# Kernel optimization log

Hardware: AMD Instinct MI355X
Metric: run time of the kernel (lower is better)

Reference implementation:

```python
import jax, jax.numpy as jnp
import numpy as np

HEADS = 16

def setup_inputs() -> dict:
    key = jax.random.key(0)
    k1, k2, k3, k4 = jax.random.split(key, 4)
    B, T, S, W = 2, 2048, 2048, 1024
    x = jax.random.normal(k1, (B, T, W), dtype=jnp.float32)
    cond_k = jax.random.normal(k2, (B, S, W), dtype=jnp.float32)
    cond_v = jax.random.normal(k3, (B, S, W), dtype=jnp.float32)
    w_proj = jax.random.normal(k4, (W, W), dtype=jnp.float32) * 0.02
    b_proj = jnp.zeros((W,), dtype=jnp.float32)
    return {"x": x, "cond_k": cond_k, "cond_v": cond_v, "w_proj": w_proj, "b_proj": b_proj}

def reference(x, cond_k, cond_v, w_proj, b_proj):
    B, T, W = x.shape
    S = cond_k.shape[1]
    H = HEADS
    d = W // H
    scale = 1.0 / jnp.sqrt(jnp.sqrt(jnp.float32(d)))  # applied to both q and k
    q = x.reshape(B, T, H, d) * scale
    k = cond_k.reshape(B, S, H, d) * scale
    v = cond_v.reshape(B, S, H, d)
    # scores: [B, H, T, S]
    scores = jnp.einsum('bthd,bshd->bhts', q, k)
    w = jax.nn.softmax(scores.astype(jnp.float32), axis=-1).astype(scores.dtype)
    out = jnp.einsum('bhts,bshd->bthd', w, v).reshape(B, T, W)
    # c_proj: torch Linear -> x @ W.T + b
    return out @ w_proj.T + b_proj
```

## Files before the change

### kernel.cpp

```cpp
#include <hip/hip_runtime.h>

#define Bn 2
#define Hn 16
#define Tn 2048
#define Sn 2048
#define Wd 1024
#define Dh 64

typedef __attribute__((ext_vector_type(8))) short s16x8;
typedef __attribute__((ext_vector_type(4))) short s16x4;
typedef __attribute__((ext_vector_type(4))) float f32x4;
typedef __attribute__((ext_vector_type(4))) unsigned u32x4;

#define MFMA(a, b, c) __builtin_amdgcn_mfma_f32_16x16x32_bf16((a), (b), (c), 0, 0, 0)

__device__ __forceinline__ s16x8 ld8(const short* p) { return *(const s16x8*)p; }

__device__ __forceinline__ short f2bf(float f) {
    unsigned u = __builtin_bit_cast(unsigned, f);
    u += 0x7FFFu + ((u >> 16) & 1u);
    return (short)(u >> 16);
}

__device__ __forceinline__ unsigned cvtpk(float lo, float hi) {
    unsigned r;
    asm("v_cvt_pk_bf16_f32 %0, %1, %2" : "=v"(r) : "v"(lo), "v"(hi));
    return r;
}

__global__ void cvt_scale(const float* __restrict__ in, short* __restrict__ out,
                          int n, float s) {
    int i = (blockIdx.x * 256 + threadIdx.x) * 8;
    if (i < n) {
        float4 a = *(const float4*)(in + i);
        float4 b = *(const float4*)(in + i + 4);
        s16x8 o;
        o[0] = f2bf(a.x * s); o[1] = f2bf(a.y * s); o[2] = f2bf(a.z * s); o[3] = f2bf(a.w * s);
        o[4] = f2bf(b.x * s); o[5] = f2bf(b.y * s); o[6] = f2bf(b.z * s); o[7] = f2bf(b.w * s);
        *(s16x8*)(out + i) = o;
    }
}

__global__ __launch_bounds__(256) void vtrans(const float* __restrict__ cv,
                                              short* __restrict__ vt) {
    __shared__ short T[64][68];
    const int st = blockIdx.x & 31;
    const int bh = blockIdx.x >> 5;
    const int b = bh >> 4, h = bh & 15;
    const int tid = threadIdx.x;
#pragma unroll
    for (int i = 0; i < 4; ++i) {
        int f = i * 256 + tid, sr = f >> 4, c4 = f & 15;
        float4 v = *(const float4*)(cv + (size_t)(b * Sn + st * 64 + sr) * Wd + h * Dh + c4 * 4);
        s16x4 o;
        o[0] = f2bf(v.x); o[1] = f2bf(v.y); o[2] = f2bf(v.z); o[3] = f2bf(v.w);
        *(s16x4*)&T[sr][c4 * 4] = o;
    }
    __syncthreads();
#pragma unroll
    for (int i = 0; i < 4; ++i) {
        int f = i * 256 + tid, dr = f >> 4, p4 = f & 15;
        s16x4 o;
#pragma unroll
        for (int k = 0; k < 4; ++k) {
            int sl = ((p4 >> 3) * 2 + (p4 & 1)) * 16 + ((p4 >> 1) & 3) * 4 + k;
            o[k] = T[sl][dr];
        }
        *(s16x4*)(vt + (size_t)(bh * Dh + dr) * Sn + st * 64 + p4 * 4) = o;
    }
}

#define KSTR 72

__global__ __launch_bounds__(256, 2) void attn_fused(
    const float* __restrict__ x, const short* __restrict__ kb,
    const short* __restrict__ vt, short* __restrict__ ao)
{
    __shared__ alignas(16) short Ks[2][64 * KSTR];
    __shared__ alignas(16) short Vs[2][64 * KSTR];

    const int tid  = threadIdx.x;
    const int w    = tid >> 6;
    const int l    = tid & 63;
    const int quad = l >> 4;
    const int l16  = l & 15;

    const int bh = blockIdx.x & 31;
    const int qt = blockIdx.x >> 5;
    const int b  = bh >> 4, h = bh & 15;

    const int qrow0 = qt * 128 + w * 32;

    const float SQ = 0.125f * 1.4426950408889634f;
    s16x8 aq[2][2];
#pragma unroll
    for (int mi = 0; mi < 2; ++mi)
#pragma unroll
        for (int c = 0; c < 2; ++c) {
            const float* p = x + (size_t)(b * Tn + qrow0 + mi * 16 + l16) * Wd
                               + h * Dh + c * 32 + quad * 8;
            float4 a = ((const float4*)p)[0], bb = ((const float4*)p)[1];
            s16x8 o;
            o[0] = f2bf(a.x * SQ); o[1] = f2bf(a.y * SQ); o[2] = f2bf(a.z * SQ); o[3] = f2bf(a.w * SQ);
            o[4] = f2bf(bb.x * SQ); o[5] = f2bf(bb.y * SQ); o[6] = f2bf(bb.z * SQ); o[7] = f2bf(bb.w * SQ);
            aq[mi][c] = o;
        }

    f32x4 oacc[2][4];
    float dn[2];
#pragma unroll
    for (int mi = 0; mi < 2; ++mi) {
#pragma unroll
        for (int nt = 0; nt < 4; ++nt) {
            oacc[mi][nt][0] = 0.f; oacc[mi][nt][1] = 0.f;
            oacc[mi][nt][2] = 0.f; oacc[mi][nt][3] = 0.f;
        }
        dn[mi] = 0.f;
    }

    const short* kb_h = kb + (size_t)(b * Sn) * Wd + h * Dh;
    const short* vt_h = vt + (size_t)(bh * Dh) * Sn;

    const int sr = tid >> 3;
    const int sg = tid & 7;

    s16x8 kr[2], vr[2];
#pragma unroll
    for (int i = 0; i < 2; ++i) {
        int r0 = sr + i * 32;
        kr[i] = ld8(kb_h + (size_t)r0 * Wd + sg * 8);
        vr[i] = ld8(vt_h + (size_t)r0 * Sn + sg * 8);
    }
#pragma unroll
    for (int i = 0; i < 2; ++i) {
        int r0 = sr + i * 32;
        *(s16x8*)&Ks[0][r0 * KSTR + sg * 8] = kr[i];
        *(s16x8*)&Vs[0][r0 * KSTR + sg * 8] = vr[i];
    }
    __syncthreads();

    const int NIT = Sn / 64;
    for (int it = 0; it < NIT; ++it) {
        const int p = it & 1;

        if (it + 1 < NIT) {
            const int s1 = (it + 1) * 64;
#pragma unroll
            for (int i = 0; i < 2; ++i) {
                int r0 = sr + i * 32;
                kr[i] = ld8(kb_h + (size_t)(s1 + r0) * Wd + sg * 8);
                vr[i] = ld8(vt_h + (size_t)r0 * Sn + s1 + sg * 8);
            }
        }

        f32x4 sc[2][4];
        const f32x4 z = {0.f, 0.f, 0.f, 0.f};
        __builtin_amdgcn_s_setprio(1);
#pragma unroll
        for (int sj = 0; sj < 4; ++sj) {
            s16x8 k0 = *(const s16x8*)&Ks[p][(sj * 16 + l16) * KSTR + quad * 8];
            s16x8 k1 = *(const s16x8*)&Ks[p][(sj * 16 + l16) * KSTR + 32 + quad * 8];
#pragma unroll
            for (int mi = 0; mi < 2; ++mi) {
                sc[mi][sj] = MFMA(k0, aq[mi][0], z);
                sc[mi][sj] = MFMA(k1, aq[mi][1], sc[mi][sj]);
            }
        }
        __builtin_amdgcn_s_setprio(0);

        s16x8 ap[2][2];
#pragma unroll
        for (int mi = 0; mi < 2; ++mi) {
            float ex[4][4];
#pragma unroll
            for (int sj = 0; sj < 4; ++sj)
#pragma unroll
                for (int r = 0; r < 4; ++r)
                    ex[sj][r] = __builtin_amdgcn_exp2f(sc[mi][sj][r]);
            dn[mi] += (((ex[0][0] + ex[0][1]) + (ex[0][2] + ex[0][3]))
                     + ((ex[1][0] + ex[1][1]) + (ex[1][2] + ex[1][3])))
                    + (((ex[2][0] + ex[2][1]) + (ex[2][2] + ex[2][3]))
                     + ((ex[3][0] + ex[3][1]) + (ex[3][2] + ex[3][3])));
#pragma unroll
            for (int g = 0; g < 2; ++g) {
                u32x4 pk;
                pk[0] = cvtpk(ex[2 * g][0],     ex[2 * g][1]);
                pk[1] = cvtpk(ex[2 * g][2],     ex[2 * g][3]);
                pk[2] = cvtpk(ex[2 * g + 1][0], ex[2 * g + 1][1]);
                pk[3] = cvtpk(ex[2 * g + 1][2], ex[2 * g + 1][3]);
                ap[mi][g] = __builtin_bit_cast(s16x8, pk);
            }
        }

        s16x8 bv[4][2];
#pragma unroll
        for (int nt = 0; nt < 4; ++nt)
#pragma unroll
            for (int g = 0; g < 2; ++g)
                bv[nt][g] = *(const s16x8*)&Vs[p][(nt * 16 + l16) * KSTR + g * 32 + quad * 8];
        __builtin_amdgcn_s_setprio(1);
#pragma unroll
        for (int mi = 0; mi < 2; ++mi)
#pragma unroll
            for (int nt = 0; nt < 4; ++nt) {
                oacc[mi][nt] = MFMA(ap[mi][0], bv[nt][0], oacc[mi][nt]);
                oacc[mi][nt] = MFMA(ap[mi][1], bv[nt][1], oacc[mi][nt]);
            }
        __builtin_amdgcn_s_setprio(0);

        if (it + 1 < NIT) {
#pragma unroll
            for (int i = 0; i < 2; ++i) {
                int r0 = sr + i * 32;
                *(s16x8*)&Ks[p ^ 1][r0 * KSTR + sg * 8] = kr[i];
                *(s16x8*)&Vs[p ^ 1][r0 * KSTR + sg * 8] = vr[i];
            }
        }
        __syncthreads();
    }

#pragma unroll
    for (int mi = 0; mi < 2; ++mi) {
        float d = dn[mi];
        d += __shfl_xor(d, 16);
        d += __shfl_xor(d, 32);
        float invl = 1.0f / d;
#pragma unroll
        for (int r = 0; r < 4; ++r) {
            float inv = __shfl(invl, quad * 4 + r);
            int t = qrow0 + mi * 16 + quad * 4 + r;
#pragma unroll
            for (int nt = 0; nt < 4; ++nt)
                ao[(size_t)(b * Tn + t) * Wd + h * Dh + nt * 16 + l16] =
                    f2bf(oacc[mi][nt][r] * inv);
        }
    }
}

#define LSTR 40

__global__ __launch_bounds__(256, 2) void proj_gemm(
    const short* __restrict__ A, const short* __restrict__ Wb,
    const float* __restrict__ bias, float* __restrict__ out)
{
    __shared__ alignas(16) short As[2][128 * LSTR];
    __shared__ alignas(16) short Bs[2][64 * LSTR];

    const int tid  = threadIdx.x;
    const int w    = tid >> 6;
    const int l    = tid & 63;
    const int quad = l >> 4;
    const int l16  = l & 15;

    const int bn = blockIdx.x & 15;
    const int bm = blockIdx.x >> 4;
    const int m0 = bm * 128;
    const int n0 = bn * 64;
    const int wm = (w & 1) * 64;
    const int wn = (w >> 1) * 32;

    const int rr = tid >> 2;
    const int sg = tid & 3;

    f32x4 acc[4][2];
#pragma unroll
    for (int mi = 0; mi < 4; ++mi)
#pragma unroll
        for (int nt = 0; nt < 2; ++nt) {
            acc[mi][nt][0] = 0.f; acc[mi][nt][1] = 0.f;
            acc[mi][nt][2] = 0.f; acc[mi][nt][3] = 0.f;
        }

    s16x8 ra0 = ld8(A  + (size_t)(m0 + rr) * Wd + sg * 8);
    s16x8 ra1 = ld8(A  + (size_t)(m0 + 64 + rr) * Wd + sg * 8);
    s16x8 rb  = ld8(Wb + (size_t)(n0 + rr) * Wd + sg * 8);
    *(s16x8*)&As[0][rr * LSTR + sg * 8]        = ra0;
    *(s16x8*)&As[0][(rr + 64) * LSTR + sg * 8] = ra1;
    *(s16x8*)&Bs[0][rr * LSTR + sg * 8]        = rb;
    __syncthreads();

    for (int k0 = 0; k0 < Wd; k0 += 32) {
        const int p = (k0 >> 5) & 1;

        if (k0 + 32 < Wd) {
            ra0 = ld8(A  + (size_t)(m0 + rr) * Wd + k0 + 32 + sg * 8);
            ra1 = ld8(A  + (size_t)(m0 + 64 + rr) * Wd + k0 + 32 + sg * 8);
            rb  = ld8(Wb + (size_t)(n0 + rr) * Wd + k0 + 32 + sg * 8);
        }

        s16x8 a[4], bw[2];
#pragma unroll
        for (int mi = 0; mi < 4; ++mi)
            a[mi] = *(const s16x8*)&As[p][(wm + mi * 16 + l16) * LSTR + quad * 8];
#pragma unroll
        for (int nt = 0; nt < 2; ++nt)
            bw[nt] = *(const s16x8*)&Bs[p][(wn + nt * 16 + l16) * LSTR + quad * 8];
        __builtin_amdgcn_s_setprio(1);
#pragma unroll
        for (int mi = 0; mi < 4; ++mi)
#pragma unroll
            for (int nt = 0; nt < 2; ++nt)
                acc[mi][nt] = MFMA(a[mi], bw[nt], acc[mi][nt]);
        __builtin_amdgcn_s_setprio(0);

        if (k0 + 32 < Wd) {
            *(s16x8*)&As[p ^ 1][rr * LSTR + sg * 8]        = ra0;
            *(s16x8*)&As[p ^ 1][(rr + 64) * LSTR + sg * 8] = ra1;
            *(s16x8*)&Bs[p ^ 1][rr * LSTR + sg * 8]        = rb;
        }
        __syncthreads();
    }

#pragma unroll
    for (int nt = 0; nt < 2; ++nt) {
        float bv = bias[n0 + wn + nt * 16 + l16];
#pragma unroll
        for (int mi = 0; mi < 4; ++mi)
#pragma unroll
            for (int r = 0; r < 4; ++r)
                out[(size_t)(m0 + wm + mi * 16 + quad * 4 + r) * Wd + n0 + wn + nt * 16 + l16] =
                    acc[mi][nt][r] + bv;
    }
}

extern "C" void kernel_launch(void* const* d_in, const int* in_sizes, int n_in,
                              void* d_out, int out_size, void* d_ws, size_t ws_size,
                              hipStream_t stream) {
    const float* x  = (const float*)d_in[0];
    const float* ck = (const float*)d_in[1];
    const float* cv = (const float*)d_in[2];
    const float* wp = (const float*)d_in[3];
    const float* bp = (const float*)d_in[4];

    const int nX = Bn * Tn * Wd;
    const int nW = Wd * Wd;

    short* kbb = (short*)d_ws;
    short* vtb = kbb + nX;
    short* wbb = vtb + nX;
    short* am  = wbb + nW;

    cvt_scale<<<dim3(nX / 2048), dim3(256), 0, stream>>>(ck, kbb, nX, 1.0f);
    cvt_scale<<<dim3(nW / 2048), dim3(256), 0, stream>>>(wp, wbb, nW, 1.0f);
    vtrans<<<dim3(1024), dim3(256), 0, stream>>>(cv, vtb);

    attn_fused<<<dim3(Bn * Hn * (Tn / 128)), dim3(256), 0, stream>>>(x, kbb, vtb, am);
    proj_gemm<<<dim3((Bn * Tn / 128) * (Wd / 64)), dim3(256), 0, stream>>>(
        am, wbb, bp, (float*)d_out);
}
```

Measured before the change: 160.4 us.

## Pre-pack K/V into MFMA fragment layout and load directly to registers

A single prep kernel now converts K, V and the projection weight to bf16, writing K and V in per-lane MFMA fragment order, and replaces three separate launches. The attention kernel drops its LDS staging and barriers and loads K/V fragments straight from global memory into registers, double-buffering K across a loop unrolled by two. The softmax denominator is now computed with an MFMA against a ones vector, which replaces the scalar sums and the final shuffles. Every wave now reads K/V from global memory or L2 on its own instead of sharing them through LDS, which multiplies global traffic. Register pressure also rises.

```diff
diff --git a/kernel.cpp b/kernel.cpp
--- a/kernel.cpp
+++ b/kernel.cpp
@@ -28,57 +28,64 @@
     return r;
 }
 
-__global__ void cvt_scale(const float* __restrict__ in, short* __restrict__ out,
-                          int n, float s) {
-    int i = (blockIdx.x * 256 + threadIdx.x) * 8;
-    if (i < n) {
-        float4 a = *(const float4*)(in + i);
-        float4 b = *(const float4*)(in + i + 4);
+__global__ __launch_bounds__(256) void prep(const float* __restrict__ ck,
+                                            const float* __restrict__ cv,
+                                            const float* __restrict__ wp,
+                                            short* __restrict__ kp,
+                                            short* __restrict__ vp,
+                                            short* __restrict__ wb)
+{
+    __shared__ short T[64][72];
+    const int blk = blockIdx.x;
+    const int tid = threadIdx.x;
+    if (blk < 2048) {
+        const int isV = blk >> 10;
+        const int c   = blk & 1023;
+        const int bh = c >> 5, sc = c & 31;
+        const int b = bh >> 4, h = bh & 15;
+        const float* src = (isV ? cv : ck) + (size_t)(b * Sn + sc * 64) * Wd + h * Dh;
+#pragma unroll
+        for (int i = 0; i < 4; ++i) {
+            int f = i * 256 + tid, sr = f >> 4, c4 = f & 15;
+            float4 v = *(const float4*)(src + (size_t)sr * Wd + c4 * 4);
+            s16x4 o;
+            o[0] = f2bf(v.x); o[1] = f2bf(v.y); o[2] = f2bf(v.z); o[3] = f2bf(v.w);
+            *(s16x4*)&T[sr][c4 * 4] = o;
+        }
+        __syncthreads();
+        const int rt = tid >> 6;
+        const int l = tid & 63, quad = l >> 4, l16 = l & 15;
+        if (!isV) {
+            size_t base = ((size_t)((bh * 128 + sc * 4 + rt) * 2)) * 512 + l * 8;
+            *(s16x8*)(kp + base)       = *(const s16x8*)&T[rt * 16 + l16][quad * 8];
+            *(s16x8*)(kp + base + 512) = *(const s16x8*)&T[rt * 16 + l16][32 + quad * 8];
+        } else {
+#pragma unroll
+            for (int g = 0; g < 2; ++g) {
+                s16x8 o;
+#pragma unroll
+                for (int j = 0; j < 8; ++j) {
+                    int s = 32 * g + 16 * (j >> 2) + quad * 4 + (j & 3);
+                    o[j] = T[s][rt * 16 + l16];
+                }
+                *(s16x8*)(vp + ((size_t)((bh * 32 + sc) * 8 + rt * 2 + g)) * 512 + l * 8) = o;
+            }
+        }
+    } else {
+        int i = ((blk - 2048) * 256 + tid) * 8;
+        float4 a = *(const float4*)(wp + i);
+        float4 b = *(const float4*)(wp + i + 4);
         s16x8 o;
-        o[0] = f2bf(a.x * s); o[1] = f2bf(a.y * s); o[2] = f2bf(a.z * s); o[3] = f2bf(a.w * s);
-        o[4] = f2bf(b.x * s); o[5] = f2bf(b.y * s); o[6] = f2bf(b.z * s); o[7] = f2bf(b.w * s);
-        *(s16x8*)(out + i) = o;
-    }
-}
-
-__global__ __launch_bounds__(256) void vtrans(const float* __restrict__ cv,
-                                              short* __restrict__ vt) {
-    __shared__ short T[64][68];
-    const int st = blockIdx.x & 31;
-    const int bh = blockIdx.x >> 5;
-    const int b = bh >> 4, h = bh & 15;
-    const int tid = threadIdx.x;
-#pragma unroll
-    for (int i = 0; i < 4; ++i) {
-        int f = i * 256 + tid, sr = f >> 4, c4 = f & 15;
-        float4 v = *(const float4*)(cv + (size_t)(b * Sn + st * 64 + sr) * Wd + h * Dh + c4 * 4);
-        s16x4 o;
-        o[0] = f2bf(v.x); o[1] = f2bf(v.y); o[2] = f2bf(v.z); o[3] = f2bf(v.w);
-        *(s16x4*)&T[sr][c4 * 4] = o;
-    }
-    __syncthreads();
-#pragma unroll
-    for (int i = 0; i < 4; ++i) {
-        int f = i * 256 + tid, dr = f >> 4, p4 = f & 15;
-        s16x4 o;
-#pragma unroll
-        for (int k = 0; k < 4; ++k) {
-            int sl = ((p4 >> 3) * 2 + (p4 & 1)) * 16 + ((p4 >> 1) & 3) * 4 + k;
-            o[k] = T[sl][dr];
-        }
-        *(s16x4*)(vt + (size_t)(bh * Dh + dr) * Sn + st * 64 + p4 * 4) = o;
-    }
-}
-
-#define KSTR 72
+        o[0] = f2bf(a.x); o[1] = f2bf(a.y); o[2] = f2bf(a.z); o[3] = f2bf(a.w);
+        o[4] = f2bf(b.x); o[5] = f2bf(b.y); o[6] = f2bf(b.z); o[7] = f2bf(b.w);
+        *(s16x8*)(wb + i) = o;
+    }
+}
 
 __global__ __launch_bounds__(256, 2) void attn_fused(
-    const float* __restrict__ x, const short* __restrict__ kb,
+    const float* __restrict__ x, const short* __restrict__ kp,
     const short* __restrict__ vt, short* __restrict__ ao)
 {
-    __shared__ alignas(16) short Ks[2][64 * KSTR];
-    __shared__ alignas(16) short Vs[2][64 * KSTR];
-
     const int tid  = threadIdx.x;
     const int w    = tid >> 6;
     const int l    = tid & 63;
@@ -106,8 +113,7 @@
             aq[mi][c] = o;
         }
 
-    f32x4 oacc[2][4];
-    float dn[2];
+    f32x4 oacc[2][4], dnacc[2];
 #pragma unroll
     for (int mi = 0; mi < 2; ++mi) {
 #pragma unroll
@@ -115,126 +121,92 @@
             oacc[mi][nt][0] = 0.f; oacc[mi][nt][1] = 0.f;
             oacc[mi][nt][2] = 0.f; oacc[mi][nt][3] = 0.f;
         }
-        dn[mi] = 0.f;
-    }
-
-    const short* kb_h = kb + (size_t)(b * Sn) * Wd + h * Dh;
-    const short* vt_h = vt + (size_t)(bh * Dh) * Sn;
-
-    const int sr = tid >> 3;
-    const int sg = tid & 7;
-
-    s16x8 kr[2], vr[2];
-#pragma unroll
-    for (int i = 0; i < 2; ++i) {
-        int r0 = sr + i * 32;
-        kr[i] = ld8(kb_h + (size_t)r0 * Wd + sg * 8);
-        vr[i] = ld8(vt_h + (size_t)r0 * Sn + sg * 8);
-    }
-#pragma unroll
-    for (int i = 0; i < 2; ++i) {
-        int r0 = sr + i * 32;
-        *(s16x8*)&Ks[0][r0 * KSTR + sg * 8] = kr[i];
-        *(s16x8*)&Vs[0][r0 * KSTR + sg * 8] = vr[i];
-    }
-    __syncthreads();
-
+        dnacc[mi][0] = 0.f; dnacc[mi][1] = 0.f; dnacc[mi][2] = 0.f; dnacc[mi][3] = 0.f;
+    }
+
+    s16x8 ones;
+#pragma unroll
+    for (int j = 0; j < 8; ++j) ones[j] = (short)0x3F80;
+
+    const short* kp_h = kp + (size_t)bh * 131072;
+    const short* vp_h = vt + (size_t)bh * 131072;
+
+    const f32x4 z = {0.f, 0.f, 0.f, 0.f};
     const int NIT = Sn / 64;
-    for (int it = 0; it < NIT; ++it) {
-        const int p = it & 1;
-
-        if (it + 1 < NIT) {
-            const int s1 = (it + 1) * 64;
-#pragma unroll
-            for (int i = 0; i < 2; ++i) {
-                int r0 = sr + i * 32;
-                kr[i] = ld8(kb_h + (size_t)(s1 + r0) * Wd + sg * 8);
-                vr[i] = ld8(vt_h + (size_t)r0 * Sn + s1 + sg * 8);
-            }
-        }
-
-        f32x4 sc[2][4];
-        const f32x4 z = {0.f, 0.f, 0.f, 0.f};
-        __builtin_amdgcn_s_setprio(1);
-#pragma unroll
-        for (int sj = 0; sj < 4; ++sj) {
-            s16x8 k0 = *(const s16x8*)&Ks[p][(sj * 16 + l16) * KSTR + quad * 8];
-            s16x8 k1 = *(const s16x8*)&Ks[p][(sj * 16 + l16) * KSTR + 32 + quad * 8];
-#pragma unroll
-            for (int mi = 0; mi < 2; ++mi) {
-                sc[mi][sj] = MFMA(k0, aq[mi][0], z);
-                sc[mi][sj] = MFMA(k1, aq[mi][1], sc[mi][sj]);
-            }
-        }
-        __builtin_amdgcn_s_setprio(0);
-
-        s16x8 ap[2][2];
-#pragma unroll
-        for (int mi = 0; mi < 2; ++mi) {
-            float ex[4][4];
-#pragma unroll
-            for (int sj = 0; sj < 4; ++sj)
-#pragma unroll
-                for (int r = 0; r < 4; ++r)
-                    ex[sj][r] = __builtin_amdgcn_exp2f(sc[mi][sj][r]);
-            dn[mi] += (((ex[0][0] + ex[0][1]) + (ex[0][2] + ex[0][3]))
-                     + ((ex[1][0] + ex[1][1]) + (ex[1][2] + ex[1][3])))
-                    + (((ex[2][0] + ex[2][1]) + (ex[2][2] + ex[2][3]))
-                     + ((ex[3][0] + ex[3][1]) + (ex[3][2] + ex[3][3])));
-#pragma unroll
-            for (int g = 0; g < 2; ++g) {
-                u32x4 pk;
-                pk[0] = cvtpk(ex[2 * g][0],     ex[2 * g][1]);
-                pk[1] = cvtpk(ex[2 * g][2],     ex[2 * g][3]);
-                pk[2] = cvtpk(ex[2 * g + 1][0], ex[2 * g + 1][1]);
-                pk[3] = cvtpk(ex[2 * g + 1][2], ex[2 * g + 1][3]);
-                ap[mi][g] = __builtin_bit_cast(s16x8, pk);
-            }
-        }
-
-        s16x8 bv[4][2];
-#pragma unroll
-        for (int nt = 0; nt < 4; ++nt)
-#pragma unroll
-            for (int g = 0; g < 2; ++g)
-                bv[nt][g] = *(const s16x8*)&Vs[p][(nt * 16 + l16) * KSTR + g * 32 + quad * 8];
-        __builtin_amdgcn_s_setprio(1);
-#pragma unroll
-        for (int mi = 0; mi < 2; ++mi)
-#pragma unroll
-            for (int nt = 0; nt < 4; ++nt) {
-                oacc[mi][nt] = MFMA(ap[mi][0], bv[nt][0], oacc[mi][nt]);
-                oacc[mi][nt] = MFMA(ap[mi][1], bv[nt][1], oacc[mi][nt]);
-            }
-        __builtin_amdgcn_s_setprio(0);
-
-        if (it + 1 < NIT) {
-#pragma unroll
-            for (int i = 0; i < 2; ++i) {
-                int r0 = sr + i * 32;
-                *(s16x8*)&Ks[p ^ 1][r0 * KSTR + sg * 8] = kr[i];
-                *(s16x8*)&Vs[p ^ 1][r0 * KSTR + sg * 8] = vr[i];
-            }
-        }
-        __syncthreads();
-    }
-
-#pragma unroll
-    for (int mi = 0; mi < 2; ++mi) {
-        float d = dn[mi];
-        d += __shfl_xor(d, 16);
-        d += __shfl_xor(d, 32);
-        float invl = 1.0f / d;
+
+    s16x8 kfA[4][2], kfB[4][2];
+#pragma unroll
+    for (int sj = 0; sj < 4; ++sj)
+#pragma unroll
+        for (int g = 0; g < 2; ++g)
+            kfA[sj][g] = ld8(kp_h + ((size_t)(sj * 2 + g)) * 512 + l * 8);
+
+#define BODY(KF, KN, itv)                                                       \
+    do {                                                                        \
+        if ((itv) + 1 < NIT) {                                                  \
+            _Pragma("unroll") for (int sj = 0; sj < 4; ++sj)                    \
+                _Pragma("unroll") for (int g = 0; g < 2; ++g)                   \
+                    KN[sj][g] = ld8(kp_h +                                      \
+                        ((size_t)(((itv) + 1) * 8 + sj * 2 + g)) * 512 + l * 8);\
+        }                                                                       \
+        s16x8 vf[4][2];                                                         \
+        _Pragma("unroll") for (int nt = 0; nt < 4; ++nt)                        \
+            _Pragma("unroll") for (int g = 0; g < 2; ++g)                       \
+                vf[nt][g] = ld8(vp_h +                                          \
+                    ((size_t)((itv) * 8 + nt * 2 + g)) * 512 + l * 8);          \
+        f32x4 sc[2][4];                                                         \
+        __builtin_amdgcn_s_setprio(1);                                          \
+        _Pragma("unroll") for (int sj = 0; sj < 4; ++sj)                        \
+            _Pragma("unroll") for (int mi = 0; mi < 2; ++mi) {                  \
+                sc[mi][sj] = MFMA(KF[sj][0], aq[mi][0], z);                     \
+                sc[mi][sj] = MFMA(KF[sj][1], aq[mi][1], sc[mi][sj]);            \
+            }                                                                   \
+        __builtin_amdgcn_s_setprio(0);                                          \
+        s16x8 ap[2][2];                                                         \
+        _Pragma("unroll") for (int mi = 0; mi < 2; ++mi) {                      \
+            float ex[4][4];                                                     \
+            _Pragma("unroll") for (int sj = 0; sj < 4; ++sj)                    \
+                _Pragma("unroll") for (int r = 0; r < 4; ++r)                   \
+                    ex[sj][r] = __builtin_amdgcn_exp2f(sc[mi][sj][r]);          \
+            _Pragma("unroll") for (int g = 0; g < 2; ++g) {                     \
+                u32x4 pk;                                                       \
+                pk[0] = cvtpk(ex[2 * g][0],     ex[2 * g][1]);                  \
+                pk[1] = cvtpk(ex[2 * g][2],     ex[2 * g][3]);                  \
+                pk[2] = cvtpk(ex[2 * g + 1][0], ex[2 * g + 1][1]);              \
+                pk[3] = cvtpk(ex[2 * g + 1][2], ex[2 * g + 1][3]);              \
+                ap[mi][g] = __builtin_bit_cast(s16x8, pk);                      \
+            }                                                                   \
+        }                                                                       \
+        __builtin_amdgcn_s_setprio(1);                                          \
+        _Pragma("unroll") for (int mi = 0; mi < 2; ++mi) {                      \
+            dnacc[mi] = MFMA(ap[mi][0], ones, dnacc[mi]);                       \
+            dnacc[mi] = MFMA(ap[mi][1], ones, dnacc[mi]);                       \
+        }                                                                       \
+        _Pragma("unroll") for (int mi = 0; mi < 2; ++mi)                        \
+            _Pragma("unroll") for (int nt = 0; nt < 4; ++nt) {                  \
+                oacc[mi][nt] = MFMA(ap[mi][0], vf[nt][0], oacc[mi][nt]);        \
+                oacc[mi][nt] = MFMA(ap[mi][1], vf[nt][1], oacc[mi][nt]);        \
+            }                                                                   \
+        __builtin_amdgcn_s_setprio(0);                                          \
+    } while (0)
+
+    for (int it = 0; it < NIT; it += 2) {
+        BODY(kfA, kfB, it);
+        BODY(kfB, kfA, it + 1);
+    }
+#undef BODY
+
+#pragma unroll
+    for (int mi = 0; mi < 2; ++mi)
 #pragma unroll
         for (int r = 0; r < 4; ++r) {
-            float inv = __shfl(invl, quad * 4 + r);
+            float inv = 1.0f / dnacc[mi][r];
             int t = qrow0 + mi * 16 + quad * 4 + r;
 #pragma unroll
             for (int nt = 0; nt < 4; ++nt)
                 ao[(size_t)(b * Tn + t) * Wd + h * Dh + nt * 16 + l16] =
                     f2bf(oacc[mi][nt][r] * inv);
         }
-    }
 }
 
 #define LSTR 40
@@ -335,16 +307,14 @@
     const int nX = Bn * Tn * Wd;
     const int nW = Wd * Wd;
 
-    short* kbb = (short*)d_ws;
-    short* vtb = kbb + nX;
-    short* wbb = vtb + nX;
+    short* kpb = (short*)d_ws;
+    short* vpb = kpb + nX;
+    short* wbb = vpb + nX;
     short* am  = wbb + nW;
 
-    cvt_scale<<<dim3(nX / 2048), dim3(256), 0, stream>>>(ck, kbb, nX, 1.0f);
-    cvt_scale<<<dim3(nW / 2048), dim3(256), 0, stream>>>(wp, wbb, nW, 1.0f);
-    vtrans<<<dim3(1024), dim3(256), 0, stream>>>(cv, vtb);
-
-    attn_fused<<<dim3(Bn * Hn * (Tn / 128)), dim3(256), 0, stream>>>(x, kbb, vtb, am);
+    prep<<<dim3(2048 + nW / 2048), dim3(256), 0, stream>>>(ck, cv, wp, kpb, vpb, wbb);
+
+    attn_fused<<<dim3(Bn * Hn * (Tn / 128)), dim3(256), 0, stream>>>(x, kpb, vpb, am);
     proj_gemm<<<dim3((Bn * Tn / 128) * (Wd / 64)), dim3(256), 0, stream>>>(
         am, wbb, bp, (float*)d_out);
 }
```

Result: faster. 155.9 us (-2.8%).
